# Kernel optimization log

Hardware: AMD Instinct MI355X
Metric: run time of the kernel (lower is better)

## Reference

```python
import jax, jax.numpy as jnp
import numpy as np

B, CH, CW, H, FH, FW = 32, 16, 16, 8, 4, 4
NQ = 64
NK = CH * FH * CW * FW  # 4096
D_IN, D_V, D_MODEL = 512, 64, 512


def setup_inputs() -> dict:
    key = jax.random.key(0)
    k1, k2, k3, k4, k5 = jax.random.split(key, 5)
    att12 = jax.random.uniform(k1, (B, CH, CW, H, FH, FW), dtype=jnp.float32)
    att3 = jax.random.uniform(k2, (B, H, NQ, CH * CW), dtype=jnp.float32)
    values = jax.random.normal(k3, (B, NK, D_IN), dtype=jnp.float32)
    # Learned params (xavier-ish scale)
    W_v = jax.random.normal(k4, (H * D_V, D_IN), dtype=jnp.float32) * (1.0 / np.sqrt(D_IN))
    b_v = jnp.zeros((H * D_V,), dtype=jnp.float32)
    W_o = jax.random.normal(k5, (D_MODEL, H * D_V), dtype=jnp.float32) * (1.0 / np.sqrt(H * D_V))
    b_o = jnp.zeros((D_MODEL,), dtype=jnp.float32)
    return {"att12": att12, "att3": att3, "values": values,
            "W_v": W_v, "b_v": b_v, "W_o": W_o, "b_o": b_o}


def reference(att12, att3, values, W_v, b_v, W_o, b_o):
    b_s, h, nq, _ = att3.shape
    ch = cw = CH
    fh, fw = att12.shape[-2:]
    nk = values.shape[1]
    d_v = W_v.shape[0] // h
    # v: [b, h, nk, d_v]
    v = (values @ W_v.T + b_v).reshape(b_s, nk, h, d_v).transpose(0, 2, 1, 3)
    # att12 -> [b, h, 1, ch, cw, fh, fw]
    a12 = jnp.transpose(att12, (0, 3, 1, 2, 4, 5))[:, :, None]
    # att3 -> [b, h, nq, ch, cw, 1, 1]
    a3 = att3.reshape(b_s, h, nq, ch, cw, 1, 1)
    # broadcast multiply, then interleave to key order (ch, fh, cw, fw)
    att = (a12 * a3).transpose(0, 1, 2, 3, 5, 4, 6).reshape(b_s, h, nq, nk)
    att = jax.nn.softmax(att, axis=-1)
    out = jnp.einsum('bhqk,bhkd->bhqd', att, v)
    out = out.transpose(0, 2, 1, 3).reshape(b_s, nq, h * d_v)
    return out @ W_o.T + b_o
```

## Files before the change

### kernel.cpp

```cpp
#include <hip/hip_runtime.h>

typedef short bf16x8 __attribute__((ext_vector_type(8)));
typedef short bf16x4 __attribute__((ext_vector_type(4)));
typedef float f32x4 __attribute__((ext_vector_type(4)));

__device__ __forceinline__ unsigned short f2bf(float f) {
  union { float f; unsigned u; } v; v.f = f;
  unsigned r = v.u + 0x7fffu + ((v.u >> 16) & 1u);
  return (unsigned short)(r >> 16);
}

__device__ __forceinline__ void gld_lds16(const void* g, void* l) {
  __builtin_amdgcn_global_load_lds(
      (const __attribute__((address_space(1))) void*)g,
      (__attribute__((address_space(3))) void*)l, 16, 0, 0);
}

__global__ __launch_bounds__(256) void convW(const float* __restrict__ in,
                                             unsigned short* __restrict__ out) {
  long i = (long)(blockIdx.x * 256 + threadIdx.x) * 4;
  f32x4 d = *(const f32x4*)(in + i);
  bf16x4 o;
  o[0] = (short)f2bf(d[0]); o[1] = (short)f2bf(d[1]);
  o[2] = (short)f2bf(d[2]); o[3] = (short)f2bf(d[3]);
  *(bf16x4*)(out + i) = o;
}

__global__ __launch_bounds__(256) void bias2_kernel(const float* __restrict__ Wo,
                                                    const float* __restrict__ b_v,
                                                    const float* __restrict__ b_o,
                                                    float* __restrict__ bias2) {
  int e = blockIdx.x * 256 + threadIdx.x;
  const float* wrow = Wo + (long)e * 512;
  float s = 0.f;
#pragma unroll 4
  for (int d = 0; d < 512; d += 4) {
    f32x4 w = *(const f32x4*)(wrow + d);
    f32x4 bv = *(const f32x4*)(b_v + d);
    s += w[0] * bv[0] + w[1] * bv[1] + w[2] * bv[2] + w[3] * bv[3];
  }
  bias2[e] = s + b_o[e];
}

__global__ __launch_bounds__(256, 2) void vt_gemm(
    const unsigned short* __restrict__ Wvb, const float* __restrict__ V,
    unsigned short* __restrict__ vT) {
  const int t = threadIdx.x, lane = t & 63, wave = t >> 6;
  const int n0 = blockIdx.x * 128;
  const int m0 = blockIdx.y * 128;
  const int b = blockIdx.z;
  const float* Vb = V + (long)b * (4096L * 512) + (long)n0 * 512;

  __shared__ __align__(16) unsigned short As[128 * 32];
  __shared__ __align__(16) unsigned short Bs[128 * 32];

  const int wm = (wave >> 1) * 64, wn = (wave & 1) * 64;
  const int l16 = lane & 15, quad = lane >> 4;
  const int brow0 = t >> 3, bc4 = (t & 7) * 4;

  f32x4 acc[4][4];
#pragma unroll
  for (int i = 0; i < 4; ++i)
#pragma unroll
    for (int j = 0; j < 4; ++j) acc[i][j] = (f32x4){0.f, 0.f, 0.f, 0.f};

  for (int k0 = 0; k0 < 512; k0 += 32) {
#pragma unroll
    for (int s = 0; s < 2; ++s) {
      int li = s * 256 + t;
      int row = li >> 2, kq = (li & 3) * 8;
      gld_lds16(Wvb + (long)(m0 + row) * 512 + k0 + kq, (char*)As + (s * 256 + wave * 64) * 16);
    }
#pragma unroll
    for (int j = 0; j < 4; ++j) {
      int row = brow0 + 32 * j;
      f32x4 d = *(const f32x4*)(Vb + (long)row * 512 + k0 + bc4);
      bf16x4 p;
      p[0] = (short)f2bf(d[0]); p[1] = (short)f2bf(d[1]);
      p[2] = (short)f2bf(d[2]); p[3] = (short)f2bf(d[3]);
      *(bf16x4*)(Bs + row * 32 + bc4) = p;
    }
    __syncthreads();
    bf16x8 af[4], bfv[4];
#pragma unroll
    for (int i = 0; i < 4; ++i)
      af[i] = *(const bf16x8*)(As + (wm + i * 16 + l16) * 32 + quad * 8);
#pragma unroll
    for (int j = 0; j < 4; ++j)
      bfv[j] = *(const bf16x8*)(Bs + (wn + j * 16 + l16) * 32 + quad * 8);
#pragma unroll
    for (int i = 0; i < 4; ++i)
#pragma unroll
      for (int j = 0; j < 4; ++j)
        acc[i][j] = __builtin_amdgcn_mfma_f32_16x16x32_bf16(af[i], bfv[j], acc[i][j], 0, 0, 0);
    __syncthreads();
  }
  unsigned short* o = vT + (long)b * 2097152;
#pragma unroll
  for (int i = 0; i < 4; ++i)
#pragma unroll
    for (int j = 0; j < 4; ++j) {
      int col = n0 + wn + j * 16 + l16;
#pragma unroll
      for (int r = 0; r < 4; ++r) {
        int row = m0 + wm + i * 16 + quad * 4 + r;
        o[(long)row * 4096 + col] = f2bf(acc[i][j][r]);
      }
    }
}

__global__ __launch_bounds__(256, 2) void o_gemm(
    const float* __restrict__ att12, const float* __restrict__ att3,
    const unsigned short* __restrict__ vT, unsigned short* __restrict__ U) {
  const int bh = blockIdx.x;
  const int b = bh >> 3, h = bh & 7;
  const int t = threadIdx.x, lane = t & 63, wave = t >> 6;

  __shared__ __align__(16) unsigned short As[4 * 64 * 32];
  __shared__ __align__(16) unsigned short Bs[4 * 64 * 32];
  __shared__ float Ored[64 * 68];
  __shared__ float Zl[4][64];
  __shared__ float rZa[64];

  const unsigned short* vTb = vT + (long)b * 2097152 + (long)h * 64 * 4096;
  const int gq = t & 63, gw = t >> 6;
  const float* a3row = att3 + ((long)bh * 64 + gq) * 256;
  const float* a12b = att12 + (long)b * 32768 + h * 16;
  const int l16 = lane & 15, quad = lane >> 4;

  f32x4 acc[4][4];
#pragma unroll
  for (int i = 0; i < 4; ++i)
#pragma unroll
    for (int j = 0; j < 4; ++j) acc[i][j] = (f32x4){0.f, 0.f, 0.f, 0.f};
  float zacc = 0.f;

  for (int it = 0; it < 32; ++it) {
#pragma unroll
    for (int s = 0; s < 4; ++s) {
      int row = t >> 2, kq = (t & 3) * 8;
      int kk = s * 1024 + it * 32 + kq;
      gld_lds16(vTb + (long)row * 4096 + kk, (char*)Bs + s * 4096 + wave * 1024);
    }
    {
      int kbase = gw * 1024 + it * 32;
      int ch = kbase >> 8, fh = (kbase >> 6) & 3, cw0 = (kbase >> 2) & 15;
      f32x4 y0 = *(const f32x4*)(a3row + ch * 16 + cw0);
      f32x4 y1 = *(const f32x4*)(a3row + ch * 16 + cw0 + 4);
      const float* ap = a12b + ch * 2048 + cw0 * 128 + fh * 4;
      bf16x8 p[4];
#pragma unroll
      for (int cw = 0; cw < 8; ++cw) {
        float y = (cw < 4) ? y0[cw] : y1[cw - 4];
        f32x4 x = *(const f32x4*)(ap + cw * 128);
#pragma unroll
        for (int fw = 0; fw < 4; ++fw) {
          float e = __expf(x[fw] * y);
          zacc += e;
          p[cw >> 1][(cw & 1) * 4 + fw] = (short)f2bf(e);
        }
      }
#pragma unroll
      for (int g = 0; g < 4; ++g)
        *(bf16x8*)(As + gw * 2048 + gq * 32 + g * 8) = p[g];
    }
    __syncthreads();
    bf16x8 af[4], bfv[4];
#pragma unroll
    for (int i = 0; i < 4; ++i)
      af[i] = *(const bf16x8*)(As + wave * 2048 + (i * 16 + l16) * 32 + quad * 8);
#pragma unroll
    for (int j = 0; j < 4; ++j)
      bfv[j] = *(const bf16x8*)(Bs + wave * 2048 + (j * 16 + l16) * 32 + quad * 8);
#pragma unroll
    for (int i = 0; i < 4; ++i)
#pragma unroll
      for (int j = 0; j < 4; ++j)
        acc[i][j] = __builtin_amdgcn_mfma_f32_16x16x32_bf16(af[i], bfv[j], acc[i][j], 0, 0, 0);
    __syncthreads();
  }

  Zl[gw][gq] = zacc;
  __syncthreads();
  if (t < 64) rZa[t] = 1.0f / (Zl[0][t] + Zl[1][t] + Zl[2][t] + Zl[3][t]);
#pragma unroll
  for (int w = 0; w < 4; ++w) {
    if (wave == w) {
#pragma unroll
      for (int i = 0; i < 4; ++i)
#pragma unroll
        for (int j = 0; j < 4; ++j) {
          int col = j * 16 + l16;
#pragma unroll
          for (int r = 0; r < 4; ++r) {
            int row = i * 16 + quad * 4 + r;
            if (w == 0) Ored[row * 68 + col] = acc[i][j][r];
            else Ored[row * 68 + col] += acc[i][j][r];
          }
        }
    }
    __syncthreads();
  }
  {
    int q = t >> 2, dv0 = (t & 3) * 16;
    float rz = rZa[q];
    unsigned short* up = U + ((long)(b * 64 + q)) * 512 + h * 64 + dv0;
    bf16x8 o0, o1;
#pragma unroll
    for (int j = 0; j < 8; ++j) o0[j] = (short)f2bf(Ored[q * 68 + dv0 + j] * rz);
#pragma unroll
    for (int j = 0; j < 8; ++j) o1[j] = (short)f2bf(Ored[q * 68 + dv0 + 8 + j] * rz);
    *(bf16x8*)(up) = o0;
    *(bf16x8*)(up + 8) = o1;
  }
}

template <int BM, int BN, bool OUT_BF16, bool ADD_BIAS>
__global__ __launch_bounds__(256, 2) void gemm_bt(
    const unsigned short* __restrict__ A, const unsigned short* __restrict__ Bt,
    void* __restrict__ C, const float* __restrict__ bias,
    int K, int lda, int ldb, int ldc) {
  constexpr int BK = 32;
  const int t = threadIdx.x;
  const int lane = t & 63;
  const int wave = t >> 6;
  const int m0 = blockIdx.y * BM;
  const int n0 = blockIdx.x * BN;

  A += (long)m0 * lda;
  Bt += (long)n0 * ldb;

  __shared__ __align__(16) unsigned short As[BM * BK];
  __shared__ __align__(16) unsigned short Bs[BN * BK];

  constexpr int TM = BM / 32;
  constexpr int TN = BN / 32;
  const int wm = (wave >> 1) * (BM / 2);
  const int wn = (wave & 1) * (BN / 2);
  const int l16 = lane & 15;
  const int quad = lane >> 4;

  f32x4 acc[TM][TN];
#pragma unroll
  for (int i = 0; i < TM; ++i)
#pragma unroll
    for (int j = 0; j < TN; ++j) acc[i][j] = (f32x4){0.f, 0.f, 0.f, 0.f};

  constexpr int ASHOT = (BM * 4) / 256;
  constexpr int BSHOT = (BN * 4) / 256;

  for (int k0 = 0; k0 < K; k0 += BK) {
#pragma unroll
    for (int s = 0; s < ASHOT; ++s) {
      int li = s * 256 + t;
      int row = li >> 2, kq = (li & 3) * 8;
      gld_lds16(A + (long)row * lda + k0 + kq, (char*)As + (s * 256 + wave * 64) * 16);
    }
#pragma unroll
    for (int s = 0; s < BSHOT; ++s) {
      int li = s * 256 + t;
      int row = li >> 2, kq = (li & 3) * 8;
      gld_lds16(Bt + (long)row * ldb + k0 + kq, (char*)Bs + (s * 256 + wave * 64) * 16);
    }
    __syncthreads();
    bf16x8 af[TM], bfv[TN];
#pragma unroll
    for (int i = 0; i < TM; ++i)
      af[i] = *(const bf16x8*)(As + (wm + i * 16 + l16) * BK + quad * 8);
#pragma unroll
    for (int j = 0; j < TN; ++j)
      bfv[j] = *(const bf16x8*)(Bs + (wn + j * 16 + l16) * BK + quad * 8);
#pragma unroll
    for (int i = 0; i < TM; ++i)
#pragma unroll
      for (int j = 0; j < TN; ++j)
        acc[i][j] = __builtin_amdgcn_mfma_f32_16x16x32_bf16(af[i], bfv[j], acc[i][j], 0, 0, 0);
    __syncthreads();
  }

#pragma unroll
  for (int i = 0; i < TM; ++i) {
#pragma unroll
    for (int j = 0; j < TN; ++j) {
      int col = wn + j * 16 + l16;
#pragma unroll
      for (int r = 0; r < 4; ++r) {
        int row = wm + i * 16 + quad * 4 + r;
        float v = acc[i][j][r];
        if (ADD_BIAS) v += bias[n0 + col];
        long idx = (long)(m0 + row) * ldc + (n0 + col);
        if (OUT_BF16) ((unsigned short*)C)[idx] = f2bf(v);
        else ((float*)C)[idx] = v;
      }
    }
  }
}

extern "C" void kernel_launch(void* const* d_in, const int* in_sizes, int n_in,
                              void* d_out, int out_size, void* d_ws, size_t ws_size,
                              hipStream_t stream) {
  const float* att12 = (const float*)d_in[0];
  const float* att3  = (const float*)d_in[1];
  const float* values = (const float*)d_in[2];
  const float* W_v = (const float*)d_in[3];
  const float* b_v = (const float*)d_in[4];
  const float* W_o = (const float*)d_in[5];
  const float* b_o = (const float*)d_in[6];
  float* out = (float*)d_out;

  char* ws = (char*)d_ws;
  unsigned short* vT    = (unsigned short*)(ws);
  unsigned short* U     = (unsigned short*)(ws + 134217728L);
  unsigned short* Wvb   = (unsigned short*)(ws + 136314880L);
  unsigned short* Wob   = (unsigned short*)(ws + 136839168L);
  float*          bias2 = (float*)(ws + 137363456L);

  convW<<<dim3(256), dim3(256), 0, stream>>>(W_v, Wvb);
  convW<<<dim3(256), dim3(256), 0, stream>>>(W_o, Wob);
  bias2_kernel<<<dim3(2), dim3(256), 0, stream>>>(W_o, b_v, b_o, bias2);

  vt_gemm<<<dim3(32, 4, 32), dim3(256), 0, stream>>>(Wvb, values, vT);

  o_gemm<<<dim3(256), dim3(256), 0, stream>>>(att12, att3, vT, U);

  gemm_bt<64, 64, false, true><<<dim3(8, 32), dim3(256), 0, stream>>>(
      U, Wob, out, bias2, 512, 512, 512, 512);

  (void)in_sizes; (void)n_in; (void)out_size; (void)ws_size;
}
```

Measured before the change: 556.3 us.

## Double-buffer LDS in vt_gemm and o_gemm and fuse prep kernels

Both main GEMM kernels move to two LDS buffers so the next tile's global loads (async LDS copies and register-staged fp32 values) are issued while MFMAs run on the current tile, which also removes one barrier per iteration. In o_gemm the exp/softmax-numerator generation for the next tile is computed after the MFMAs to overlap with them. The three small setup kernels are merged into one launch, and bf16 packing switches to a perm-based round-half-up pack. This costs twice the LDS and more live registers, which may lower occupancy, and the rounding differs slightly from round-to-nearest-even.

New measurement: 551.3 us. No clear change (-0.9%).

```diff
diff --git a/kernel.cpp b/kernel.cpp
--- a/kernel.cpp
+++ b/kernel.cpp
@@ -3,6 +3,8 @@
 typedef short bf16x8 __attribute__((ext_vector_type(8)));
 typedef short bf16x4 __attribute__((ext_vector_type(4)));
 typedef float f32x4 __attribute__((ext_vector_type(4)));
+typedef unsigned int u32x2 __attribute__((ext_vector_type(2)));
+typedef unsigned int u32x4 __attribute__((ext_vector_type(4)));
 
 __device__ __forceinline__ unsigned short f2bf(float f) {
   union { float f; unsigned u; } v; v.f = f;
@@ -10,36 +12,44 @@
   return (unsigned short)(r >> 16);
 }
 
+__device__ __forceinline__ unsigned int pk2(float a, float b) {
+  union { float f; unsigned u; } x, y; x.f = a; y.f = b;
+  return __builtin_amdgcn_perm(y.u + 0x8000u, x.u + 0x8000u, 0x07060302u);
+}
+
 __device__ __forceinline__ void gld_lds16(const void* g, void* l) {
   __builtin_amdgcn_global_load_lds(
       (const __attribute__((address_space(1))) void*)g,
       (__attribute__((address_space(3))) void*)l, 16, 0, 0);
 }
 
-__global__ __launch_bounds__(256) void convW(const float* __restrict__ in,
-                                             unsigned short* __restrict__ out) {
-  long i = (long)(blockIdx.x * 256 + threadIdx.x) * 4;
-  f32x4 d = *(const f32x4*)(in + i);
-  bf16x4 o;
-  o[0] = (short)f2bf(d[0]); o[1] = (short)f2bf(d[1]);
-  o[2] = (short)f2bf(d[2]); o[3] = (short)f2bf(d[3]);
-  *(bf16x4*)(out + i) = o;
-}
-
-__global__ __launch_bounds__(256) void bias2_kernel(const float* __restrict__ Wo,
-                                                    const float* __restrict__ b_v,
-                                                    const float* __restrict__ b_o,
-                                                    float* __restrict__ bias2) {
-  int e = blockIdx.x * 256 + threadIdx.x;
-  const float* wrow = Wo + (long)e * 512;
-  float s = 0.f;
+__global__ __launch_bounds__(256) void prep(const float* __restrict__ W_v,
+                                            const float* __restrict__ W_o,
+                                            const float* __restrict__ b_v,
+                                            const float* __restrict__ b_o,
+                                            unsigned short* __restrict__ Wvb,
+                                            unsigned short* __restrict__ Wob,
+                                            float* __restrict__ bias2) {
+  int bid = blockIdx.x;
+  if (bid < 512) {
+    const float* in = (bid < 256) ? W_v : W_o;
+    unsigned short* out = (bid < 256) ? Wvb : Wob;
+    long i = (long)((bid & 255) * 256 + threadIdx.x) * 4;
+    f32x4 d = *(const f32x4*)(in + i);
+    u32x2 w; w[0] = pk2(d[0], d[1]); w[1] = pk2(d[2], d[3]);
+    *(u32x2*)(out + i) = w;
+  } else {
+    int e = (bid - 512) * 256 + threadIdx.x;
+    const float* wrow = W_o + (long)e * 512;
+    float s = 0.f;
 #pragma unroll 4
-  for (int d = 0; d < 512; d += 4) {
-    f32x4 w = *(const f32x4*)(wrow + d);
-    f32x4 bv = *(const f32x4*)(b_v + d);
-    s += w[0] * bv[0] + w[1] * bv[1] + w[2] * bv[2] + w[3] * bv[3];
-  }
-  bias2[e] = s + b_o[e];
+    for (int d = 0; d < 512; d += 4) {
+      f32x4 w = *(const f32x4*)(wrow + d);
+      f32x4 bv = *(const f32x4*)(b_v + d);
+      s += w[0] * bv[0] + w[1] * bv[1] + w[2] * bv[2] + w[3] * bv[3];
+    }
+    bias2[e] = s + b_o[e];
+  }
 }
 
 __global__ __launch_bounds__(256, 2) void vt_gemm(
@@ -51,50 +61,66 @@
   const int b = blockIdx.z;
   const float* Vb = V + (long)b * (4096L * 512) + (long)n0 * 512;
 
-  __shared__ __align__(16) unsigned short As[128 * 32];
-  __shared__ __align__(16) unsigned short Bs[128 * 32];
+  __shared__ __align__(16) unsigned short As[2][128 * 32];
+  __shared__ __align__(16) unsigned short Bs[2][128 * 32];
 
   const int wm = (wave >> 1) * 64, wn = (wave & 1) * 64;
   const int l16 = lane & 15, quad = lane >> 4;
   const int brow0 = t >> 3, bc4 = (t & 7) * 4;
 
-  f32x4 acc[4][4];
-#pragma unroll
-  for (int i = 0; i < 4; ++i)
-#pragma unroll
-    for (int j = 0; j < 4; ++j) acc[i][j] = (f32x4){0.f, 0.f, 0.f, 0.f};
-
-  for (int k0 = 0; k0 < 512; k0 += 32) {
+  f32x4 breg[4];
+  auto loadB = [&](int k0) {
+#pragma unroll
+    for (int j = 0; j < 4; ++j)
+      breg[j] = *(const f32x4*)(Vb + (long)(brow0 + 32 * j) * 512 + k0 + bc4);
+  };
+  auto asyncA = [&](int k0, int buf) {
 #pragma unroll
     for (int s = 0; s < 2; ++s) {
       int li = s * 256 + t;
       int row = li >> 2, kq = (li & 3) * 8;
-      gld_lds16(Wvb + (long)(m0 + row) * 512 + k0 + kq, (char*)As + (s * 256 + wave * 64) * 16);
-    }
+      gld_lds16(Wvb + (long)(m0 + row) * 512 + k0 + kq,
+                (char*)&As[buf][0] + (s * 256 + wave * 64) * 16);
+    }
+  };
+
+  f32x4 acc[4][4];
+#pragma unroll
+  for (int i = 0; i < 4; ++i)
+#pragma unroll
+    for (int j = 0; j < 4; ++j) acc[i][j] = (f32x4){0.f, 0.f, 0.f, 0.f};
+
+  asyncA(0, 0);
+  loadB(0);
+
+  for (int r = 0; r < 16; ++r) {
+    const int buf = r & 1;
 #pragma unroll
     for (int j = 0; j < 4; ++j) {
-      int row = brow0 + 32 * j;
-      f32x4 d = *(const f32x4*)(Vb + (long)row * 512 + k0 + bc4);
-      bf16x4 p;
-      p[0] = (short)f2bf(d[0]); p[1] = (short)f2bf(d[1]);
-      p[2] = (short)f2bf(d[2]); p[3] = (short)f2bf(d[3]);
-      *(bf16x4*)(Bs + row * 32 + bc4) = p;
-    }
-    __syncthreads();
+      u32x2 w;
+      w[0] = pk2(breg[j][0], breg[j][1]);
+      w[1] = pk2(breg[j][2], breg[j][3]);
+      *(u32x2*)(&Bs[buf][(brow0 + 32 * j) * 32 + bc4]) = w;
+    }
+    __syncthreads();
+    if (r < 15) {
+      loadB((r + 1) * 32);
+      asyncA((r + 1) * 32, buf ^ 1);
+    }
     bf16x8 af[4], bfv[4];
 #pragma unroll
     for (int i = 0; i < 4; ++i)
-      af[i] = *(const bf16x8*)(As + (wm + i * 16 + l16) * 32 + quad * 8);
-#pragma unroll
-    for (int j = 0; j < 4; ++j)
-      bfv[j] = *(const bf16x8*)(Bs + (wn + j * 16 + l16) * 32 + quad * 8);
+      af[i] = *(const bf16x8*)(&As[buf][(wm + i * 16 + l16) * 32 + quad * 8]);
+#pragma unroll
+    for (int j = 0; j < 4; ++j)
+      bfv[j] = *(const bf16x8*)(&Bs[buf][(wn + j * 16 + l16) * 32 + quad * 8]);
 #pragma unroll
     for (int i = 0; i < 4; ++i)
 #pragma unroll
       for (int j = 0; j < 4; ++j)
         acc[i][j] = __builtin_amdgcn_mfma_f32_16x16x32_bf16(af[i], bfv[j], acc[i][j], 0, 0, 0);
-    __syncthreads();
-  }
+  }
+
   unsigned short* o = vT + (long)b * 2097152;
 #pragma unroll
   for (int i = 0; i < 4; ++i)
@@ -116,8 +142,8 @@
   const int b = bh >> 3, h = bh & 7;
   const int t = threadIdx.x, lane = t & 63, wave = t >> 6;
 
-  __shared__ __align__(16) unsigned short As[4 * 64 * 32];
-  __shared__ __align__(16) unsigned short Bs[4 * 64 * 32];
+  __shared__ __align__(16) unsigned short As[2][4 * 64 * 32];
+  __shared__ __align__(16) unsigned short Bs[2][4 * 64 * 32];
   __shared__ float Ored[64 * 68];
   __shared__ float Zl[4][64];
   __shared__ float rZa[64];
@@ -135,49 +161,59 @@
     for (int j = 0; j < 4; ++j) acc[i][j] = (f32x4){0.f, 0.f, 0.f, 0.f};
   float zacc = 0.f;
 
-  for (int it = 0; it < 32; ++it) {
+  unsigned int pk[16];
+  auto genexp = [&](int r) {
+    int kbase = gw * 1024 + r * 32;
+    int ch = kbase >> 8, fh = (kbase >> 6) & 3, cw0 = (kbase >> 2) & 15;
+    f32x4 y0 = *(const f32x4*)(a3row + ch * 16 + cw0);
+    f32x4 y1 = *(const f32x4*)(a3row + ch * 16 + cw0 + 4);
+    const float* ap = a12b + ch * 2048 + cw0 * 128 + fh * 4;
+#pragma unroll
+    for (int cw = 0; cw < 8; ++cw) {
+      float y = (cw < 4) ? y0[cw] : y1[cw - 4];
+      f32x4 x = *(const f32x4*)(ap + cw * 128);
+      float e0 = __expf(x[0] * y), e1 = __expf(x[1] * y);
+      float e2 = __expf(x[2] * y), e3 = __expf(x[3] * y);
+      zacc += (e0 + e1) + (e2 + e3);
+      pk[cw * 2] = pk2(e0, e1);
+      pk[cw * 2 + 1] = pk2(e2, e3);
+    }
+  };
+  auto asyncB = [&](int r, int buf) {
 #pragma unroll
     for (int s = 0; s < 4; ++s) {
       int row = t >> 2, kq = (t & 3) * 8;
-      int kk = s * 1024 + it * 32 + kq;
-      gld_lds16(vTb + (long)row * 4096 + kk, (char*)Bs + s * 4096 + wave * 1024);
-    }
+      int kk = s * 1024 + r * 32 + kq;
+      gld_lds16(vTb + (long)row * 4096 + kk, (char*)&Bs[buf][0] + s * 4096 + wave * 1024);
+    }
+  };
+
+  asyncB(0, 0);
+  genexp(0);
+
+  for (int r = 0; r < 32; ++r) {
+    const int buf = r & 1;
     {
-      int kbase = gw * 1024 + it * 32;
-      int ch = kbase >> 8, fh = (kbase >> 6) & 3, cw0 = (kbase >> 2) & 15;
-      f32x4 y0 = *(const f32x4*)(a3row + ch * 16 + cw0);
-      f32x4 y1 = *(const f32x4*)(a3row + ch * 16 + cw0 + 4);
-      const float* ap = a12b + ch * 2048 + cw0 * 128 + fh * 4;
-      bf16x8 p[4];
-#pragma unroll
-      for (int cw = 0; cw < 8; ++cw) {
-        float y = (cw < 4) ? y0[cw] : y1[cw - 4];
-        f32x4 x = *(const f32x4*)(ap + cw * 128);
-#pragma unroll
-        for (int fw = 0; fw < 4; ++fw) {
-          float e = __expf(x[fw] * y);
-          zacc += e;
-          p[cw >> 1][(cw & 1) * 4 + fw] = (short)f2bf(e);
-        }
-      }
+      unsigned short* dst = &As[buf][gw * 2048 + gq * 32];
 #pragma unroll
       for (int g = 0; g < 4; ++g)
-        *(bf16x8*)(As + gw * 2048 + gq * 32 + g * 8) = p[g];
-    }
-    __syncthreads();
+        *(u32x4*)(dst + g * 8) = (u32x4){pk[g * 4], pk[g * 4 + 1], pk[g * 4 + 2], pk[g * 4 + 3]};
+    }
+    __syncthreads();
+    if (r < 31) asyncB(r + 1, buf ^ 1);
     bf16x8 af[4], bfv[4];
 #pragma unroll
     for (int i = 0; i < 4; ++i)
-      af[i] = *(const bf16x8*)(As + wave * 2048 + (i * 16 + l16) * 32 + quad * 8);
-#pragma unroll
-    for (int j = 0; j < 4; ++j)
-      bfv[j] = *(const bf16x8*)(Bs + wave * 2048 + (j * 16 + l16) * 32 + quad * 8);
+      af[i] = *(const bf16x8*)(&As[buf][wave * 2048 + (i * 16 + l16) * 32 + quad * 8]);
+#pragma unroll
+    for (int j = 0; j < 4; ++j)
+      bfv[j] = *(const bf16x8*)(&Bs[buf][wave * 2048 + (j * 16 + l16) * 32 + quad * 8]);
 #pragma unroll
     for (int i = 0; i < 4; ++i)
 #pragma unroll
       for (int j = 0; j < 4; ++j)
         acc[i][j] = __builtin_amdgcn_mfma_f32_16x16x32_bf16(af[i], bfv[j], acc[i][j], 0, 0, 0);
-    __syncthreads();
+    if (r < 31) genexp(r + 1);
   }
 
   Zl[gw][gq] = zacc;
@@ -192,10 +228,10 @@
         for (int j = 0; j < 4; ++j) {
           int col = j * 16 + l16;
 #pragma unroll
-          for (int r = 0; r < 4; ++r) {
-            int row = i * 16 + quad * 4 + r;
-            if (w == 0) Ored[row * 68 + col] = acc[i][j][r];
-            else Ored[row * 68 + col] += acc[i][j][r];
+          for (int rr = 0; rr < 4; ++rr) {
+            int row = i * 16 + quad * 4 + rr;
+            if (w == 0) Ored[row * 68 + col] = acc[i][j][rr];
+            else Ored[row * 68 + col] += acc[i][j][rr];
           }
         }
     }
@@ -205,20 +241,22 @@
     int q = t >> 2, dv0 = (t & 3) * 16;
     float rz = rZa[q];
     unsigned short* up = U + ((long)(b * 64 + q)) * 512 + h * 64 + dv0;
-    bf16x8 o0, o1;
-#pragma unroll
-    for (int j = 0; j < 8; ++j) o0[j] = (short)f2bf(Ored[q * 68 + dv0 + j] * rz);
-#pragma unroll
-    for (int j = 0; j < 8; ++j) o1[j] = (short)f2bf(Ored[q * 68 + dv0 + 8 + j] * rz);
-    *(bf16x8*)(up) = o0;
-    *(bf16x8*)(up + 8) = o1;
-  }
-}
-
-template <int BM, int BN, bool OUT_BF16, bool ADD_BIAS>
+    u32x4 o0, o1;
+#pragma unroll
+    for (int j = 0; j < 4; ++j)
+      o0[j] = pk2(Ored[q * 68 + dv0 + 2 * j] * rz, Ored[q * 68 + dv0 + 2 * j + 1] * rz);
+#pragma unroll
+    for (int j = 0; j < 4; ++j)
+      o1[j] = pk2(Ored[q * 68 + dv0 + 8 + 2 * j] * rz, Ored[q * 68 + dv0 + 9 + 2 * j] * rz);
+    *(u32x4*)(up) = o0;
+    *(u32x4*)(up + 8) = o1;
+  }
+}
+
+template <int BM, int BN>
 __global__ __launch_bounds__(256, 2) void gemm_bt(
     const unsigned short* __restrict__ A, const unsigned short* __restrict__ Bt,
-    void* __restrict__ C, const float* __restrict__ bias,
+    float* __restrict__ C, const float* __restrict__ bias,
     int K, int lda, int ldb, int ldc) {
   constexpr int BK = 32;
   const int t = threadIdx.x;
@@ -286,11 +324,7 @@
 #pragma unroll
       for (int r = 0; r < 4; ++r) {
         int row = wm + i * 16 + quad * 4 + r;
-        float v = acc[i][j][r];
-        if (ADD_BIAS) v += bias[n0 + col];
-        long idx = (long)(m0 + row) * ldc + (n0 + col);
-        if (OUT_BF16) ((unsigned short*)C)[idx] = f2bf(v);
-        else ((float*)C)[idx] = v;
+        C[(long)(m0 + row) * ldc + (n0 + col)] = acc[i][j][r] + bias[n0 + col];
       }
     }
   }
@@ -315,15 +349,13 @@
   unsigned short* Wob   = (unsigned short*)(ws + 136839168L);
   float*          bias2 = (float*)(ws + 137363456L);
 
-  convW<<<dim3(256), dim3(256), 0, stream>>>(W_v, Wvb);
-  convW<<<dim3(256), dim3(256), 0, stream>>>(W_o, Wob);
-  bias2_kernel<<<dim3(2), dim3(256), 0, stream>>>(W_o, b_v, b_o, bias2);
+  prep<<<dim3(514), dim3(256), 0, stream>>>(W_v, W_o, b_v, b_o, Wvb, Wob, bias2);
 
   vt_gemm<<<dim3(32, 4, 32), dim3(256), 0, stream>>>(Wvb, values, vT);
 
   o_gemm<<<dim3(256), dim3(256), 0, stream>>>(att12, att3, vT, U);
 
-  gemm_bt<64, 64, false, true><<<dim3(8, 32), dim3(256), 0, stream>>>(
+  gemm_bt<64, 64><<<dim3(8, 32), dim3(256), 0, stream>>>(
       U, Wob, out, bias2, 512, 512, 512, 512);
 
   (void)in_sizes; (void)n_in; (void)out_size; (void)ws_size;
```
